# Kernel tuning notes

Measured on AMD Instinct MI355X. Metric: run time of the kernel, lower is better.

## Reference

```python
import jax, jax.numpy as jnp
import numpy as np

B, H, SEQLEN, HEAD_DIM = 1, 16, 4096, 64
SCALE = 1.0 / float(np.sqrt(HEAD_DIM))


def setup_inputs() -> dict:
    key = jax.random.key(0)
    kq, kk, kv = jax.random.split(key, 3)
    q = jax.random.normal(kq, (B, H, SEQLEN, HEAD_DIM), dtype=jnp.float32)
    k = jax.random.normal(kk, (B, H, HEAD_DIM, SEQLEN), dtype=jnp.float32)  # pre-transposed
    v = jax.random.normal(kv, (B, H, SEQLEN, HEAD_DIM), dtype=jnp.float32)
    return {"q": q, "k": k, "v": v}


def reference(q, k, v):
    # causal additive mask: -inf strictly above the diagonal
    mask = jnp.where(
        jnp.triu(jnp.ones((SEQLEN, SEQLEN), dtype=bool), k=1),
        jnp.float32(-jnp.inf), jnp.float32(0.0),
    ).astype(q.dtype)
    scores = jnp.einsum('bhsd,bhdt->bhst', q, k) * SCALE + mask  # [B,H,S,S]
    row_max = jnp.max(scores, axis=-1, keepdims=True)
    p_exp = jnp.exp(scores - row_max)
    denom = jnp.sum(p_exp, axis=-1, keepdims=True)
    p = p_exp / denom                                            # softmax probs
    out = jnp.einsum('bhst,bhtd->bhsd', p, v)                    # [B,H,S,D]
    row_sum = jnp.sum(p, axis=2)                                 # per-key accumulated attention [B,H,S]
    return (out, row_sum)
```

## Files before the change

kernel.cpp:

```cpp
#include <hip/hip_runtime.h>
#include <hip/hip_bf16.h>

#define HEADS 16
#define SEQ   4096
#define DIM   64
#define QT    64
#define KT    64
#define SCALE 0.125f
#define CF    0.18033688011112042f
#define LOG2E 1.4426950408889634f

typedef __bf16 v8bf  __attribute__((ext_vector_type(8)));
typedef __bf16 v4bf  __attribute__((ext_vector_type(4)));
typedef float  f32x4 __attribute__((ext_vector_type(4)));

__device__ __forceinline__ __bf16 to_bf(float f) { return (__bf16)f; }
__device__ __forceinline__ float ex2(float x) { return __builtin_amdgcn_exp2f(x); }
__device__ __forceinline__ float lg2(float x) { return __builtin_amdgcn_logf(x); }

__device__ __forceinline__ void gload16(const __bf16* g, __bf16* l) {
    __builtin_amdgcn_global_load_lds(
        (const __attribute__((address_space(1))) void*)g,
        (__attribute__((address_space(3))) void*)l,
        16, 0, 0);
}

__global__ __launch_bounds__(256) void conv_fused_kernel(
    const float* __restrict__ qg, const float* __restrict__ kg,
    const float* __restrict__ vg, __bf16* __restrict__ Qb,
    __bf16* __restrict__ Kb, __bf16* __restrict__ Vb)
{
    __shared__ __bf16 ldsT[64][65];
    const int h   = blockIdx.y;
    const int t0  = blockIdx.x * 64;
    const int tid = threadIdx.x;
    const int rr  = tid >> 2;
    const int cq  = (tid & 3) * 16;

    if (blockIdx.z == 2) {
        const float* src = qg + ((size_t)h * SEQ + t0 + rr) * DIM + cq;
        __bf16* dst = Qb + ((size_t)h * SEQ + t0 + rr) * DIM + cq;
        v8bf o0, o1;
        #pragma unroll
        for (int j = 0; j < 2; ++j) {
            float4 f0 = *(const float4*)(src + 8 * j);
            float4 f1 = *(const float4*)(src + 8 * j + 4);
            v8bf o;
            o[0] = to_bf(f0.x * CF); o[1] = to_bf(f0.y * CF);
            o[2] = to_bf(f0.z * CF); o[3] = to_bf(f0.w * CF);
            o[4] = to_bf(f1.x * CF); o[5] = to_bf(f1.y * CF);
            o[6] = to_bf(f1.z * CF); o[7] = to_bf(f1.w * CF);
            if (j == 0) o0 = o; else o1 = o;
        }
        *(v8bf*)dst = o0;
        *(v8bf*)(dst + 8) = o1;
        return;
    }

    if (blockIdx.z == 0) {
        const float* src = kg + ((size_t)h * DIM + rr) * SEQ + t0 + cq;
        #pragma unroll
        for (int j = 0; j < 4; ++j) {
            float4 f = *(const float4*)(src + 4 * j);
            ldsT[rr][cq + 4 * j + 0] = to_bf(f.x);
            ldsT[rr][cq + 4 * j + 1] = to_bf(f.y);
            ldsT[rr][cq + 4 * j + 2] = to_bf(f.z);
            ldsT[rr][cq + 4 * j + 3] = to_bf(f.w);
        }
        __syncthreads();
        __bf16* dst = Kb + (size_t)h * SEQ * DIM + (size_t)(t0 + rr) * DIM + cq;
        v8bf o0, o1;
        #pragma unroll
        for (int i = 0; i < 8; ++i) {
            o0[i] = ldsT[cq + i][rr];
            o1[i] = ldsT[cq + 8 + i][rr];
        }
        *(v8bf*)dst = o0;
        *(v8bf*)(dst + 8) = o1;
    } else {
        const float* src = vg + ((size_t)h * SEQ + t0 + rr) * DIM + cq;
        #pragma unroll
        for (int j = 0; j < 4; ++j) {
            float4 f = *(const float4*)(src + 4 * j);
            ldsT[rr][cq + 4 * j + 0] = to_bf(f.x);
            ldsT[rr][cq + 4 * j + 1] = to_bf(f.y);
            ldsT[rr][cq + 4 * j + 2] = to_bf(f.z);
            ldsT[rr][cq + 4 * j + 3] = to_bf(f.w);
        }
        __syncthreads();
        __bf16* dst0 = Vb + ((size_t)h * DIM + rr) * SEQ + t0;
        const int n  = cq >> 4;
        const int c0 = 32 * (n >> 1) + 4 * (n & 1);
        #pragma unroll
        for (int j2 = 0; j2 < 4; ++j2) {
            v4bf ch;
            #pragma unroll
            for (int r = 0; r < 4; ++r)
                ch[r] = ldsT[cq + 4 * j2 + r][rr];
            *(v4bf*)(dst0 + c0 + 8 * j2) = ch;
        }
    }
}

__global__ __launch_bounds__(256, 2) void fa_fwd2_kernel(
    const __bf16* __restrict__ Qb, const __bf16* __restrict__ Kb,
    const __bf16* __restrict__ Vb, float* __restrict__ outg,
    float* __restrict__ lseg)
{
    const int b    = blockIdx.x;
    const int xcd  = b & 7;
    const int j    = b >> 3;
    const int h    = 2 * xcd + (j & 1);
    const int a    = j >> 1;
    const int tid  = threadIdx.x;
    const int wave = tid >> 6;
    const int lane = tid & 63;
    const int g    = lane >> 4;
    const int l16  = lane & 15;
    const int wit  = wave * 16 + l16;

    const int na  = a + 1;
    const int nb  = 64 - a;
    const int nIt = (nb + 1) >> 1;

    __shared__ alignas(16) __bf16 ldsK[2][2][KT * DIM];
    __shared__ alignas(16) __bf16 ldsV[2][2][DIM * KT];

    const int r0 = tid >> 3;
    const int c0 = tid & 7;
    const size_t kOff0 = (size_t)r0 * DIM + (size_t)((c0 ^ (r0 & 7)) << 3);
    const size_t kOff1 = (size_t)(r0 + 32) * DIM + (size_t)((c0 ^ ((r0 + 32) & 7)) << 3);
    const size_t vOff0 = (size_t)r0 * SEQ + (size_t)((c0 ^ (r0 & 7)) << 3);
    const size_t vOff1 = (size_t)(r0 + 32) * SEQ + (size_t)((c0 ^ ((r0 + 32) & 7)) << 3);
    const __bf16* KbH = Kb + (size_t)h * SEQ * DIM;
    const __bf16* VbH = Vb + (size_t)h * DIM * SEQ;
    const int ldsW = wave * 512;

    const int qlo = a * QT + wit;
    const int qhi = (63 - a) * QT + wit;

    const __bf16* qlr = Qb + ((size_t)h * SEQ + qlo) * DIM + g * 8;
    const __bf16* qhr = Qb + ((size_t)h * SEQ + qhi) * DIM + g * 8;
    v8bf aqlo0 = *(const v8bf*)qlr;
    v8bf aqlo1 = *(const v8bf*)(qlr + 32);
    v8bf aqhi0 = *(const v8bf*)qhr;
    v8bf aqhi1 = *(const v8bf*)(qhr + 32);

    f32x4 accl[4], acch[4];
    #pragma unroll
    for (int n = 0; n < 4; ++n) {
        accl[n] = (f32x4){0.f, 0.f, 0.f, 0.f};
        acch[n] = (f32x4){0.f, 0.f, 0.f, 0.f};
    }
    float lpl[4] = {0.f, 0.f, 0.f, 0.f};
    float lph[4] = {0.f, 0.f, 0.f, 0.f};

    int cur = 0;
    #pragma unroll
    for (int u = 0; u < 2; ++u) {
        const __bf16* kb = KbH + (size_t)(64 * u) * DIM;
        const __bf16* vb = VbH + 64 * u;
        gload16(kb + kOff0, &ldsK[0][u][ldsW]);
        gload16(kb + kOff1, &ldsK[0][u][2048 + ldsW]);
        gload16(vb + vOff0, &ldsV[0][u][ldsW]);
        gload16(vb + vOff1, &ldsV[0][u][2048 + ldsW]);
    }
    __syncthreads();

    auto sub_full = [&](int u, int t) {
        f32x4 sl[4], sh[4];
        #pragma unroll
        for (int n = 0; n < 4; ++n) {
            sl[n] = (f32x4){0.f, 0.f, 0.f, 0.f};
            sh[n] = (f32x4){0.f, 0.f, 0.f, 0.f};
        }
        __builtin_amdgcn_s_setprio(1);
        #pragma unroll
        for (int kk = 0; kk < 2; ++kk) {
            #pragma unroll
            for (int n = 0; n < 4; ++n) {
                int row  = 16 * n + l16;
                int byte = row * 128 + kk * 64 + g * 16;
                byte ^= (row & 7) << 4;
                v8bf ak = *(const v8bf*)&ldsK[cur][u][byte >> 1];
                sl[n] = __builtin_amdgcn_mfma_f32_16x16x32_bf16(
                    ak, kk ? aqlo1 : aqlo0, sl[n], 0, 0, 0);
                sh[n] = __builtin_amdgcn_mfma_f32_16x16x32_bf16(
                    ak, kk ? aqhi1 : aqhi0, sh[n], 0, 0, 0);
            }
        }
        __builtin_amdgcn_s_setprio(0);
        if (t >= na - 1) {
            const int lim = (a - t) * 64 + wit;
            #pragma unroll
            for (int n = 0; n < 4; ++n)
                #pragma unroll
                for (int r = 0; r < 4; ++r)
                    if (16 * n + 4 * g + r > lim) sl[n][r] = -3.0e38f;
        }
        v8bf pl0, pl1, ph0, ph1;
        #pragma unroll
        for (int n = 0; n < 4; ++n) {
            #pragma unroll
            for (int r = 0; r < 4; ++r) {
                float p = ex2(sl[n][r]);
                float q = ex2(sh[n][r]);
                lpl[r] += p;
                lph[r] += q;
                if (n < 2) { pl0[(n & 1) * 4 + r] = to_bf(p);
                             ph0[(n & 1) * 4 + r] = to_bf(q); }
                else       { pl1[(n & 1) * 4 + r] = to_bf(p);
                             ph1[(n & 1) * 4 + r] = to_bf(q); }
            }
        }
        __builtin_amdgcn_s_setprio(1);
        #pragma unroll
        for (int kk = 0; kk < 2; ++kk) {
            #pragma unroll
            for (int n = 0; n < 4; ++n) {
                int row  = 16 * n + l16;
                int byte = row * 128 + kk * 64 + g * 16;
                byte ^= (row & 7) << 4;
                v8bf av = *(const v8bf*)&ldsV[cur][u][byte >> 1];
                accl[n] = __builtin_amdgcn_mfma_f32_16x16x32_bf16(
                    av, kk ? pl1 : pl0, accl[n], 0, 0, 0);
                acch[n] = __builtin_amdgcn_mfma_f32_16x16x32_bf16(
                    av, kk ? ph1 : ph0, acch[n], 0, 0, 0);
            }
        }
        __builtin_amdgcn_s_setprio(0);
    };

    auto sub_hi = [&](int u, int t) {
        f32x4 sh[4];
        #pragma unroll
        for (int n = 0; n < 4; ++n) sh[n] = (f32x4){0.f, 0.f, 0.f, 0.f};
        __builtin_amdgcn_s_setprio(1);
        #pragma unroll
        for (int kk = 0; kk < 2; ++kk) {
            #pragma unroll
            for (int n = 0; n < 4; ++n) {
                int row  = 16 * n + l16;
                int byte = row * 128 + kk * 64 + g * 16;
                byte ^= (row & 7) << 4;
                v8bf ak = *(const v8bf*)&ldsK[cur][u][byte >> 1];
                sh[n] = __builtin_amdgcn_mfma_f32_16x16x32_bf16(
                    ak, kk ? aqhi1 : aqhi0, sh[n], 0, 0, 0);
            }
        }
        __builtin_amdgcn_s_setprio(0);
        if (t >= nb - 1) {
            const int lim = (63 - a - t) * 64 + wit;
            #pragma unroll
            for (int n = 0; n < 4; ++n)
                #pragma unroll
                for (int r = 0; r < 4; ++r)
                    if (16 * n + 4 * g + r > lim) sh[n][r] = -3.0e38f;
        }
        v8bf ph0, ph1;
        #pragma unroll
        for (int n = 0; n < 4; ++n) {
            #pragma unroll
            for (int r = 0; r < 4; ++r) {
                float q = ex2(sh[n][r]);
                lph[r] += q;
                if (n < 2) ph0[(n & 1) * 4 + r] = to_bf(q);
                else       ph1[(n & 1) * 4 + r] = to_bf(q);
            }
        }
        __builtin_amdgcn_s_setprio(1);
        #pragma unroll
        for (int kk = 0; kk < 2; ++kk) {
            #pragma unroll
            for (int n = 0; n < 4; ++n) {
                int row  = 16 * n + l16;
                int byte = row * 128 + kk * 64 + g * 16;
                byte ^= (row & 7) << 4;
                v8bf av = *(const v8bf*)&ldsV[cur][u][byte >> 1];
                acch[n] = __builtin_amdgcn_mfma_f32_16x16x32_bf16(
                    av, kk ? ph1 : ph0, acch[n], 0, 0, 0);
            }
        }
        __builtin_amdgcn_s_setprio(0);
    };

    #pragma unroll 1
    for (int it = 0; it < nIt; ++it) {
        if (it + 1 < nIt) {
            #pragma unroll
            for (int u = 0; u < 2; ++u) {
                const __bf16* kb = KbH + (size_t)(128 * (it + 1) + 64 * u) * DIM;
                const __bf16* vb = VbH + 128 * (it + 1) + 64 * u;
                gload16(kb + kOff0, &ldsK[cur ^ 1][u][ldsW]);
                gload16(kb + kOff1, &ldsK[cur ^ 1][u][2048 + ldsW]);
                gload16(vb + vOff0, &ldsV[cur ^ 1][u][ldsW]);
                gload16(vb + vOff1, &ldsV[cur ^ 1][u][2048 + ldsW]);
            }
        }
        const int t0 = 2 * it;
        if (t0 < na) { sub_full(0, t0); sub_full(1, t0 + 1); }
        else         { sub_hi(0, t0);   sub_hi(1, t0 + 1);   }
        __syncthreads();
        cur ^= 1;
    }

    {
        float l = (lpl[0] + lpl[1]) + (lpl[2] + lpl[3]);
        l += __shfl_xor(l, 16);
        l += __shfl_xor(l, 32);
        const float inv = 1.0f / l;
        float* orow = outg + ((size_t)h * SEQ + qlo) * DIM;
        #pragma unroll
        for (int n = 0; n < 4; ++n) {
            f32x4 o = accl[n];
            o[0] *= inv; o[1] *= inv; o[2] *= inv; o[3] *= inv;
            *(f32x4*)(orow + 16 * n + 4 * g) = o;
        }
        if (g == 0) lseg[h * SEQ + qlo] = lg2(l);
    }
    {
        float l = (lph[0] + lph[1]) + (lph[2] + lph[3]);
        l += __shfl_xor(l, 16);
        l += __shfl_xor(l, 32);
        const float inv = 1.0f / l;
        float* orow = outg + ((size_t)h * SEQ + qhi) * DIM;
        #pragma unroll
        for (int n = 0; n < 4; ++n) {
            f32x4 o = acch[n];
            o[0] *= inv; o[1] *= inv; o[2] *= inv; o[3] *= inv;
            *(f32x4*)(orow + 16 * n + 4 * g) = o;
        }
        if (g == 0) lseg[h * SEQ + qhi] = lg2(l);
    }
}

__global__ __launch_bounds__(256, 2) void fa_colsum2_kernel(
    const __bf16* __restrict__ Qb, const __bf16* __restrict__ Kb,
    const float* __restrict__ lseg, float* __restrict__ rsg)
{
    const int b    = blockIdx.x;
    const int xcd  = b & 7;
    const int j    = b >> 3;
    const int h    = 2 * xcd + (j & 1);
    const int ta   = j >> 1;
    const int tb   = 63 - ta;
    const int tid  = threadIdx.x;
    const int wave = tid >> 6;
    const int lane = tid & 63;
    const int g    = lane >> 4;
    const int l16  = lane & 15;

    __shared__ alignas(16) __bf16 ldsK2[2][KT * DIM];
    __shared__ float cs[2][4][KT];

    const int r0 = tid >> 3;
    const int c0 = tid & 7;
    const size_t kOff0 = (size_t)r0 * DIM + (size_t)((c0 ^ (r0 & 7)) << 3);
    const size_t kOff1 = (size_t)(r0 + 32) * DIM + (size_t)((c0 ^ ((r0 + 32) & 7)) << 3);
    const __bf16* KbH = Kb + (size_t)h * SEQ * DIM;
    const int ldsW = wave * 512;

    gload16(KbH + (size_t)ta * KT * DIM + kOff0, &ldsK2[0][ldsW]);
    gload16(KbH + (size_t)ta * KT * DIM + kOff1, &ldsK2[0][2048 + ldsW]);
    gload16(KbH + (size_t)tb * KT * DIM + kOff0, &ldsK2[1][ldsW]);
    gload16(KbH + (size_t)tb * KT * DIM + kOff1, &ldsK2[1][2048 + ldsW]);
    __syncthreads();

    float accA[4] = {0.f, 0.f, 0.f, 0.f};
    float accB[4] = {0.f, 0.f, 0.f, 0.f};

    #pragma unroll 1
    for (int qt = ta; qt < SEQ / QT; ++qt) {
        const int qw = qt * QT + wave * 16;
        const __bf16* qrow = Qb + ((size_t)h * SEQ + qw + l16) * DIM + g * 8;
        v8bf aq0 = *(const v8bf*)qrow;
        v8bf aq1 = *(const v8bf*)(qrow + 32);
        float4 lse4 = *(const float4*)(lseg + (size_t)h * SEQ + qw + 4 * g);

        {
            f32x4 s[4];
            #pragma unroll
            for (int n = 0; n < 4; ++n) s[n] = (f32x4){0.f, 0.f, 0.f, 0.f};
            __builtin_amdgcn_s_setprio(1);
            #pragma unroll
            for (int kk = 0; kk < 2; ++kk)
                #pragma unroll
                for (int n = 0; n < 4; ++n) {
                    int row  = 16 * n + l16;
                    int byte = row * 128 + kk * 64 + g * 16;
                    byte ^= (row & 7) << 4;
                    v8bf bk = *(const v8bf*)&ldsK2[0][byte >> 1];
                    s[n] = __builtin_amdgcn_mfma_f32_16x16x32_bf16(
                        kk ? aq1 : aq0, bk, s[n], 0, 0, 0);
                }
            __builtin_amdgcn_s_setprio(0);
            if (qt == ta) {
                #pragma unroll
                for (int n = 0; n < 4; ++n) {
                    const int key = ta * KT + 16 * n + l16;
                    #pragma unroll
                    for (int r = 0; r < 4; ++r) {
                        float e = ex2(s[n][r] - lse4[r]);
                        accA[n] += (key <= qw + 4 * g + r) ? e : 0.f;
                    }
                }
            } else {
                #pragma unroll
                for (int n = 0; n < 4; ++n)
                    #pragma unroll
                    for (int r = 0; r < 4; ++r)
                        accA[n] += ex2(s[n][r] - lse4[r]);
            }
        }
        if (qt >= tb) {
            f32x4 s[4];
            #pragma unroll
            for (int n = 0; n < 4; ++n) s[n] = (f32x4){0.f, 0.f, 0.f, 0.f};
            __builtin_amdgcn_s_setprio(1);
            #pragma unroll
            for (int kk = 0; kk < 2; ++kk)
                #pragma unroll
                for (int n = 0; n < 4; ++n) {
                    int row  = 16 * n + l16;
                    int byte = row * 128 + kk * 64 + g * 16;
                    byte ^= (row & 7) << 4;
                    v8bf bk = *(const v8bf*)&ldsK2[1][byte >> 1];
                    s[n] = __builtin_amdgcn_mfma_f32_16x16x32_bf16(
                        kk ? aq1 : aq0, bk, s[n], 0, 0, 0);
                }
            __builtin_amdgcn_s_setprio(0);
            if (qt == tb) {
                #pragma unroll
                for (int n = 0; n < 4; ++n) {
                    const int key = tb * KT + 16 * n + l16;
                    #pragma unroll
                    for (int r = 0; r < 4; ++r) {
                        float e = ex2(s[n][r] - lse4[r]);
                        accB[n] += (key <= qw + 4 * g + r) ? e : 0.f;
                    }
                }
            } else {
                #pragma unroll
                for (int n = 0; n < 4; ++n)
                    #pragma unroll
                    for (int r = 0; r < 4; ++r)
                        accB[n] += ex2(s[n][r] - lse4[r]);
            }
        }
    }

    #pragma unroll
    for (int n = 0; n < 4; ++n) {
        accA[n] += __shfl_xor(accA[n], 16);
        accA[n] += __shfl_xor(accA[n], 32);
        accB[n] += __shfl_xor(accB[n], 16);
        accB[n] += __shfl_xor(accB[n], 32);
    }
    if (lane < 16) {
        #pragma unroll
        for (int n = 0; n < 4; ++n) {
            cs[0][wave][16 * n + lane] = accA[n];
            cs[1][wave][16 * n + lane] = accB[n];
        }
    }
    __syncthreads();
    if (tid < KT) {
        rsg[(size_t)h * SEQ + ta * KT + tid] =
            cs[0][0][tid] + cs[0][1][tid] + cs[0][2][tid] + cs[0][3][tid];
    } else if (tid < 2 * KT) {
        const int t = tid - KT;
        rsg[(size_t)h * SEQ + tb * KT + t] =
            cs[1][0][t] + cs[1][1][t] + cs[1][2][t] + cs[1][3][t];
    }
}

__global__ __launch_bounds__(256, 1) void fa_fwd_v1_kernel(
    const float* __restrict__ qg, const float* __restrict__ kg,
    const float* __restrict__ vg, float* __restrict__ outg,
    float* __restrict__ lseg)
{
    const int h    = blockIdx.y;
    const int q0   = blockIdx.x * QT;
    const int tid  = threadIdx.x;
    const int wave = tid >> 6;
    const int lane = tid & 63;
    const int g    = lane >> 4;
    const int l16  = lane & 15;

    __shared__ alignas(16) __bf16 ldsK[KT * DIM];
    __shared__ alignas(16) __bf16 ldsV[DIM * KT];
    __shared__ alignas(16) __bf16 ldsP[4][16 * 72];

    const int qw = q0 + wave * 16;
    v8bf aq[2];
    {
        const float* qrow = qg + ((size_t)h * SEQ + qw + l16) * DIM;
        #pragma unroll
        for (int kk = 0; kk < 2; ++kk) {
            const float* p = qrow + kk * 32 + g * 8;
            float4 f0 = *(const float4*)p;
            float4 f1 = *(const float4*)(p + 4);
            aq[kk][0] = to_bf(f0.x); aq[kk][1] = to_bf(f0.y);
            aq[kk][2] = to_bf(f0.z); aq[kk][3] = to_bf(f0.w);
            aq[kk][4] = to_bf(f1.x); aq[kk][5] = to_bf(f1.y);
            aq[kk][6] = to_bf(f1.z); aq[kk][7] = to_bf(f1.w);
        }
    }
    f32x4 acc[4];
    #pragma unroll
    for (int n = 0; n < 4; ++n) acc[n] = (f32x4){0.f, 0.f, 0.f, 0.f};
    float m_r[4], l_r[4];
    #pragma unroll
    for (int r = 0; r < 4; ++r) { m_r[r] = -__builtin_inff(); l_r[r] = 0.f; }

    const int ntiles = q0 / KT + 1;
    const int kd = tid >> 2;
    const int kc = (tid & 3) * 16;

    for (int t = 0; t < ntiles; ++t) {
        const int t0 = t * KT;
        __syncthreads();
        {
            const float* src = kg + ((size_t)h * DIM + kd) * SEQ + t0 + kc;
            #pragma unroll
            for (int j = 0; j < 4; ++j) {
                float4 f = *(const float4*)(src + 4 * j);
                #pragma unroll
                for (int i = 0; i < 4; ++i) {
                    int row  = kc + 4 * j + i;
                    int byte = row * 128 + kd * 2;
                    byte ^= (row & 7) << 4;
                    ldsK[byte >> 1] = to_bf(((const float*)&f)[i]);
                }
            }
        }
        {
            const float* src = vg + ((size_t)h * SEQ + t0 + kd) * DIM + kc;
            #pragma unroll
            for (int j = 0; j < 4; ++j) {
                float4 f = *(const float4*)(src + 4 * j);
                #pragma unroll
                for (int i = 0; i < 4; ++i) {
                    int row  = kc + 4 * j + i;
                    int byte = row * 128 + kd * 2;
                    byte ^= (row & 7) << 4;
                    ldsV[byte >> 1] = to_bf(((const float*)&f)[i]);
                }
            }
        }
        __syncthreads();

        f32x4 s[4];
        #pragma unroll
        for (int n = 0; n < 4; ++n) s[n] = (f32x4){0.f, 0.f, 0.f, 0.f};
        #pragma unroll
        for (int kk = 0; kk < 2; ++kk)
            #pragma unroll
            for (int n = 0; n < 4; ++n) {
                int row  = 16 * n + l16;
                int byte = row * 128 + kk * 64 + g * 16;
                byte ^= (row & 7) << 4;
                v8bf bk = *(const v8bf*)&ldsK[byte >> 1];
                s[n] = __builtin_amdgcn_mfma_f32_16x16x32_bf16(aq[kk], bk, s[n], 0, 0, 0);
            }
        float pvv[4][4];
        #pragma unroll
        for (int r = 0; r < 4; ++r) {
            const int qq = qw + 4 * g + r;
            float sv[4];
            #pragma unroll
            for (int n = 0; n < 4; ++n) {
                int key = t0 + 16 * n + l16;
                sv[n] = (key <= qq) ? s[n][r] * (SCALE * LOG2E) : -3.0e38f;
            }
            float mx = fmaxf(fmaxf(sv[0], sv[1]), fmaxf(sv[2], sv[3]));
            mx = fmaxf(mx, __shfl_xor(mx, 1));
            mx = fmaxf(mx, __shfl_xor(mx, 2));
            mx = fmaxf(mx, __shfl_xor(mx, 4));
            mx = fmaxf(mx, __shfl_xor(mx, 8));
            float mnew = fmaxf(m_r[r], mx);
            float corr = ex2(m_r[r] - mnew);
            m_r[r] = mnew;
            float rs = 0.f;
            #pragma unroll
            for (int n = 0; n < 4; ++n) {
                float p = (sv[n] > -1.0e38f) ? ex2(sv[n] - mnew) : 0.f;
                pvv[n][r] = p;
                rs += p;
            }
            rs += __shfl_xor(rs, 1);
            rs += __shfl_xor(rs, 2);
            rs += __shfl_xor(rs, 4);
            rs += __shfl_xor(rs, 8);
            l_r[r] = l_r[r] * corr + rs;
            #pragma unroll
            for (int n = 0; n < 4; ++n) acc[n][r] *= corr;
        }
        #pragma unroll
        for (int n = 0; n < 4; ++n)
            #pragma unroll
            for (int r = 0; r < 4; ++r)
                ldsP[wave][(4 * g + r) * 72 + 16 * n + l16] = to_bf(pvv[n][r]);
        asm volatile("s_waitcnt lgkmcnt(0)" ::: "memory");
        __builtin_amdgcn_sched_barrier(0);
        #pragma unroll
        for (int kk = 0; kk < 2; ++kk) {
            v8bf ap = *(const v8bf*)&ldsP[wave][l16 * 72 + 32 * kk + 8 * g];
            #pragma unroll
            for (int n = 0; n < 4; ++n) {
                int row  = 16 * n + l16;
                int byte = row * 128 + kk * 64 + g * 16;
                byte ^= (row & 7) << 4;
                v8bf bv = *(const v8bf*)&ldsV[byte >> 1];
                acc[n] = __builtin_amdgcn_mfma_f32_16x16x32_bf16(ap, bv, acc[n], 0, 0, 0);
            }
        }
    }
    #pragma unroll
    for (int r = 0; r < 4; ++r) {
        const int qq  = qw + 4 * g + r;
        const float inv = 1.0f / l_r[r];
        float* orow = outg + ((size_t)h * SEQ + qq) * DIM;
        #pragma unroll
        for (int n = 0; n < 4; ++n)
            orow[16 * n + l16] = acc[n][r] * inv;
        if (l16 == 0)
            lseg[h * SEQ + qq] = m_r[r] + lg2(l_r[r]);
    }
}

__global__ __launch_bounds__(256, 1) void fa_colsum_v1_kernel(
    const float* __restrict__ qg, const float* __restrict__ kg,
    const float* __restrict__ lseg, float* __restrict__ rsg)
{
    const int h    = blockIdx.y;
    const int t0   = blockIdx.x * KT;
    const int tid  = threadIdx.x;
    const int wave = tid >> 6;
    const int lane = tid & 63;
    const int g    = lane >> 4;
    const int l16  = lane & 15;

    __shared__ alignas(16) __bf16 ldsK[KT * DIM];
    __shared__ float cs[4][KT];
    {
        const int kd = tid >> 2;
        const int kc = (tid & 3) * 16;
        const float* src = kg + ((size_t)h * DIM + kd) * SEQ + t0 + kc;
        #pragma unroll
        for (int j = 0; j < 4; ++j) {
            float4 f = *(const float4*)(src + 4 * j);
            #pragma unroll
            for (int i = 0; i < 4; ++i) {
                int row  = kc + 4 * j + i;
                int byte = row * 128 + kd * 2;
                byte ^= (row & 7) << 4;
                ldsK[byte >> 1] = to_bf(((const float*)&f)[i]);
            }
        }
    }
    __syncthreads();
    float colacc[4] = {0.f, 0.f, 0.f, 0.f};
    for (int qt = t0 / QT; qt < SEQ / QT; ++qt) {
        const int qw = qt * QT + wave * 16;
        const float* qrow = qg + ((size_t)h * SEQ + qw + l16) * DIM;
        v8bf aq[2];
        #pragma unroll
        for (int kk = 0; kk < 2; ++kk) {
            const float* p = qrow + kk * 32 + g * 8;
            float4 f0 = *(const float4*)p;
            float4 f1 = *(const float4*)(p + 4);
            aq[kk][0] = to_bf(f0.x); aq[kk][1] = to_bf(f0.y);
            aq[kk][2] = to_bf(f0.z); aq[kk][3] = to_bf(f0.w);
            aq[kk][4] = to_bf(f1.x); aq[kk][5] = to_bf(f1.y);
            aq[kk][6] = to_bf(f1.z); aq[kk][7] = to_bf(f1.w);
        }
        float lse_r[4];
        #pragma unroll
        for (int r = 0; r < 4; ++r)
            lse_r[r] = lseg[h * SEQ + qw + 4 * g + r];
        f32x4 s[4];
        #pragma unroll
        for (int n = 0; n < 4; ++n) s[n] = (f32x4){0.f, 0.f, 0.f, 0.f};
        #pragma unroll
        for (int kk = 0; kk < 2; ++kk)
            #pragma unroll
            for (int n = 0; n < 4; ++n) {
                int row  = 16 * n + l16;
                int byte = row * 128 + kk * 64 + g * 16;
                byte ^= (row & 7) << 4;
                v8bf bk = *(const v8bf*)&ldsK[byte >> 1];
                s[n] = __builtin_amdgcn_mfma_f32_16x16x32_bf16(aq[kk], bk, s[n], 0, 0, 0);
            }
        #pragma unroll
        for (int n = 0; n < 4; ++n) {
            const int key = t0 + 16 * n + l16;
            #pragma unroll
            for (int r = 0; r < 4; ++r) {
                const int qq = qw + 4 * g + r;
                if (key <= qq)
                    colacc[n] += ex2(s[n][r] * (SCALE * LOG2E) - lse_r[r]);
            }
        }
    }
    #pragma unroll
    for (int n = 0; n < 4; ++n) {
        colacc[n] += __shfl_xor(colacc[n], 16);
        colacc[n] += __shfl_xor(colacc[n], 32);
    }
    if (lane < 16) {
        #pragma unroll
        for (int n = 0; n < 4; ++n)
            cs[wave][16 * n + lane] = colacc[n];
    }
    __syncthreads();
    if (tid < KT) {
        float v = cs[0][tid] + cs[1][tid] + cs[2][tid] + cs[3][tid];
        rsg[h * SEQ + t0 + tid] = v;
    }
}

extern "C" void kernel_launch(void* const* d_in, const int* in_sizes, int n_in,
                              void* d_out, int out_size, void* d_ws, size_t ws_size,
                              hipStream_t stream) {
    (void)in_sizes; (void)n_in; (void)out_size;
    const float* qg = (const float*)d_in[0];
    const float* kg = (const float*)d_in[1];
    const float* vg = (const float*)d_in[2];
    float* outg = (float*)d_out;
    float* rsg  = outg + (size_t)HEADS * SEQ * DIM;

    const size_t nElem   = (size_t)HEADS * SEQ * DIM;
    const size_t lseB    = (size_t)HEADS * SEQ * sizeof(float);
    const size_t needB   = lseB + 3 * nElem * sizeof(__bf16);

    if (ws_size >= needB) {
        float*  lseg = (float*)d_ws;
        __bf16* Qb = (__bf16*)((char*)d_ws + lseB);
        __bf16* Kb = Qb + nElem;
        __bf16* Vb = Kb + nElem;
        conv_fused_kernel<<<dim3(SEQ / 64, HEADS, 3), 256, 0, stream>>>(
            qg, kg, vg, Qb, Kb, Vb);
        fa_fwd2_kernel<<<dim3(512), 256, 0, stream>>>(Qb, Kb, Vb, outg, lseg);
        fa_colsum2_kernel<<<dim3(512), 256, 0, stream>>>(Qb, Kb, lseg, rsg);
    } else {
        float* lseg = (float*)d_ws;
        dim3 grid(SEQ / QT, HEADS);
        fa_fwd_v1_kernel<<<grid, 256, 0, stream>>>(qg, kg, vg, outg, lseg);
        fa_colsum_v1_kernel<<<grid, 256, 0, stream>>>(qg, kg, lseg, rsg);
    }
}
```

Before: 99.99 us.

## Split key tiles across two wave groups in forward kernel with LDS reduction

The forward kernel moves from 4 to 8 waves per block. The two wave groups each process alternate 64-key tiles of the same 128-key chunk instead of one group handling both sequentially. Partial output accumulators and row sums are exchanged through LDS and combined at the end, with each group writing one of the two query tiles. This aims to raise parallelism and occupancy per CU, at the cost of an extra LDS reduction, a barrier, and tighter register limits from the 512-thread launch bound.

```diff
diff --git a/kernel.cpp b/kernel.cpp
--- a/kernel.cpp
+++ b/kernel.cpp
@@ -102,7 +102,7 @@
     }
 }
 
-__global__ __launch_bounds__(256, 2) void fa_fwd2_kernel(
+__global__ __launch_bounds__(512, 4) void fa_fwd8_kernel(
     const __bf16* __restrict__ Qb, const __bf16* __restrict__ Kb,
     const __bf16* __restrict__ Vb, float* __restrict__ outg,
     float* __restrict__ lseg)
@@ -117,30 +117,29 @@
     const int lane = tid & 63;
     const int g    = lane >> 4;
     const int l16  = lane & 15;
-    const int wit  = wave * 16 + l16;
-
-    const int na  = a + 1;
-    const int nb  = 64 - a;
-    const int nIt = (nb + 1) >> 1;
-
-    __shared__ alignas(16) __bf16 ldsK[2][2][KT * DIM];
-    __shared__ alignas(16) __bf16 ldsV[2][2][DIM * KT];
+    const int grp  = wave >> 2;
+    const int w4   = wave & 3;
+    const int wit  = w4 * 16 + l16;
+
+    const int qlo = a;
+    const int qhi = 63 - a;
+    const int NT  = 64 - a;
+    const int nIt = (NT + 1) >> 1;
+
+    __shared__ alignas(16) __bf16 ldsPool[32768];
 
     const int r0 = tid >> 3;
     const int c0 = tid & 7;
-    const size_t kOff0 = (size_t)r0 * DIM + (size_t)((c0 ^ (r0 & 7)) << 3);
-    const size_t kOff1 = (size_t)(r0 + 32) * DIM + (size_t)((c0 ^ ((r0 + 32) & 7)) << 3);
-    const size_t vOff0 = (size_t)r0 * SEQ + (size_t)((c0 ^ (r0 & 7)) << 3);
-    const size_t vOff1 = (size_t)(r0 + 32) * SEQ + (size_t)((c0 ^ ((r0 + 32) & 7)) << 3);
+    const size_t kOff = (size_t)r0 * DIM + (size_t)((c0 ^ (r0 & 7)) << 3);
+    const size_t vOff = (size_t)r0 * SEQ + (size_t)((c0 ^ (r0 & 7)) << 3);
     const __bf16* KbH = Kb + (size_t)h * SEQ * DIM;
     const __bf16* VbH = Vb + (size_t)h * DIM * SEQ;
     const int ldsW = wave * 512;
 
-    const int qlo = a * QT + wit;
-    const int qhi = (63 - a) * QT + wit;
-
-    const __bf16* qlr = Qb + ((size_t)h * SEQ + qlo) * DIM + g * 8;
-    const __bf16* qhr = Qb + ((size_t)h * SEQ + qhi) * DIM + g * 8;
+    const int qLoRow = qlo * QT + wit;
+    const int qHiRow = qhi * QT + wit;
+    const __bf16* qlr = Qb + ((size_t)h * SEQ + qLoRow) * DIM + g * 8;
+    const __bf16* qhr = Qb + ((size_t)h * SEQ + qHiRow) * DIM + g * 8;
     v8bf aqlo0 = *(const v8bf*)qlr;
     v8bf aqlo1 = *(const v8bf*)(qlr + 32);
     v8bf aqhi0 = *(const v8bf*)qhr;
@@ -158,180 +157,207 @@
     int cur = 0;
     #pragma unroll
     for (int u = 0; u < 2; ++u) {
-        const __bf16* kb = KbH + (size_t)(64 * u) * DIM;
-        const __bf16* vb = VbH + 64 * u;
-        gload16(kb + kOff0, &ldsK[0][u][ldsW]);
-        gload16(kb + kOff1, &ldsK[0][u][2048 + ldsW]);
-        gload16(vb + vOff0, &ldsV[0][u][ldsW]);
-        gload16(vb + vOff1, &ldsV[0][u][2048 + ldsW]);
+        gload16(KbH + (size_t)(64 * u) * DIM + kOff,
+                ldsPool + (size_t)u * 4096 + ldsW);
+        gload16(VbH + 64 * u + vOff,
+                ldsPool + 16384 + (size_t)u * 4096 + ldsW);
     }
     __syncthreads();
-
-    auto sub_full = [&](int u, int t) {
-        f32x4 sl[4], sh[4];
-        #pragma unroll
-        for (int n = 0; n < 4; ++n) {
-            sl[n] = (f32x4){0.f, 0.f, 0.f, 0.f};
-            sh[n] = (f32x4){0.f, 0.f, 0.f, 0.f};
-        }
-        __builtin_amdgcn_s_setprio(1);
-        #pragma unroll
-        for (int kk = 0; kk < 2; ++kk) {
-            #pragma unroll
-            for (int n = 0; n < 4; ++n) {
-                int row  = 16 * n + l16;
-                int byte = row * 128 + kk * 64 + g * 16;
-                byte ^= (row & 7) << 4;
-                v8bf ak = *(const v8bf*)&ldsK[cur][u][byte >> 1];
-                sl[n] = __builtin_amdgcn_mfma_f32_16x16x32_bf16(
-                    ak, kk ? aqlo1 : aqlo0, sl[n], 0, 0, 0);
-                sh[n] = __builtin_amdgcn_mfma_f32_16x16x32_bf16(
-                    ak, kk ? aqhi1 : aqhi0, sh[n], 0, 0, 0);
-            }
-        }
-        __builtin_amdgcn_s_setprio(0);
-        if (t >= na - 1) {
-            const int lim = (a - t) * 64 + wit;
-            #pragma unroll
-            for (int n = 0; n < 4; ++n)
-                #pragma unroll
-                for (int r = 0; r < 4; ++r)
-                    if (16 * n + 4 * g + r > lim) sl[n][r] = -3.0e38f;
-        }
-        v8bf pl0, pl1, ph0, ph1;
-        #pragma unroll
-        for (int n = 0; n < 4; ++n) {
-            #pragma unroll
-            for (int r = 0; r < 4; ++r) {
-                float p = ex2(sl[n][r]);
-                float q = ex2(sh[n][r]);
-                lpl[r] += p;
-                lph[r] += q;
-                if (n < 2) { pl0[(n & 1) * 4 + r] = to_bf(p);
-                             ph0[(n & 1) * 4 + r] = to_bf(q); }
-                else       { pl1[(n & 1) * 4 + r] = to_bf(p);
-                             ph1[(n & 1) * 4 + r] = to_bf(q); }
-            }
-        }
-        __builtin_amdgcn_s_setprio(1);
-        #pragma unroll
-        for (int kk = 0; kk < 2; ++kk) {
-            #pragma unroll
-            for (int n = 0; n < 4; ++n) {
-                int row  = 16 * n + l16;
-                int byte = row * 128 + kk * 64 + g * 16;
-                byte ^= (row & 7) << 4;
-                v8bf av = *(const v8bf*)&ldsV[cur][u][byte >> 1];
-                accl[n] = __builtin_amdgcn_mfma_f32_16x16x32_bf16(
-                    av, kk ? pl1 : pl0, accl[n], 0, 0, 0);
-                acch[n] = __builtin_amdgcn_mfma_f32_16x16x32_bf16(
-                    av, kk ? ph1 : ph0, acch[n], 0, 0, 0);
-            }
-        }
-        __builtin_amdgcn_s_setprio(0);
-    };
-
-    auto sub_hi = [&](int u, int t) {
-        f32x4 sh[4];
-        #pragma unroll
-        for (int n = 0; n < 4; ++n) sh[n] = (f32x4){0.f, 0.f, 0.f, 0.f};
-        __builtin_amdgcn_s_setprio(1);
-        #pragma unroll
-        for (int kk = 0; kk < 2; ++kk) {
-            #pragma unroll
-            for (int n = 0; n < 4; ++n) {
-                int row  = 16 * n + l16;
-                int byte = row * 128 + kk * 64 + g * 16;
-                byte ^= (row & 7) << 4;
-                v8bf ak = *(const v8bf*)&ldsK[cur][u][byte >> 1];
-                sh[n] = __builtin_amdgcn_mfma_f32_16x16x32_bf16(
-                    ak, kk ? aqhi1 : aqhi0, sh[n], 0, 0, 0);
-            }
-        }
-        __builtin_amdgcn_s_setprio(0);
-        if (t >= nb - 1) {
-            const int lim = (63 - a - t) * 64 + wit;
-            #pragma unroll
-            for (int n = 0; n < 4; ++n)
-                #pragma unroll
-                for (int r = 0; r < 4; ++r)
-                    if (16 * n + 4 * g + r > lim) sh[n][r] = -3.0e38f;
-        }
-        v8bf ph0, ph1;
-        #pragma unroll
-        for (int n = 0; n < 4; ++n) {
-            #pragma unroll
-            for (int r = 0; r < 4; ++r) {
-                float q = ex2(sh[n][r]);
-                lph[r] += q;
-                if (n < 2) ph0[(n & 1) * 4 + r] = to_bf(q);
-                else       ph1[(n & 1) * 4 + r] = to_bf(q);
-            }
-        }
-        __builtin_amdgcn_s_setprio(1);
-        #pragma unroll
-        for (int kk = 0; kk < 2; ++kk) {
-            #pragma unroll
-            for (int n = 0; n < 4; ++n) {
-                int row  = 16 * n + l16;
-                int byte = row * 128 + kk * 64 + g * 16;
-                byte ^= (row & 7) << 4;
-                v8bf av = *(const v8bf*)&ldsV[cur][u][byte >> 1];
-                acch[n] = __builtin_amdgcn_mfma_f32_16x16x32_bf16(
-                    av, kk ? ph1 : ph0, acch[n], 0, 0, 0);
-            }
-        }
-        __builtin_amdgcn_s_setprio(0);
-    };
 
     #pragma unroll 1
     for (int it = 0; it < nIt; ++it) {
         if (it + 1 < nIt) {
+            const int nbuf = cur ^ 1;
             #pragma unroll
             for (int u = 0; u < 2; ++u) {
-                const __bf16* kb = KbH + (size_t)(128 * (it + 1) + 64 * u) * DIM;
-                const __bf16* vb = VbH + 128 * (it + 1) + 64 * u;
-                gload16(kb + kOff0, &ldsK[cur ^ 1][u][ldsW]);
-                gload16(kb + kOff1, &ldsK[cur ^ 1][u][2048 + ldsW]);
-                gload16(vb + vOff0, &ldsV[cur ^ 1][u][ldsW]);
-                gload16(vb + vOff1, &ldsV[cur ^ 1][u][2048 + ldsW]);
-            }
-        }
-        const int t0 = 2 * it;
-        if (t0 < na) { sub_full(0, t0); sub_full(1, t0 + 1); }
-        else         { sub_hi(0, t0);   sub_hi(1, t0 + 1);   }
+                gload16(KbH + (size_t)(128 * (it + 1) + 64 * u) * DIM + kOff,
+                        ldsPool + (size_t)(nbuf * 2 + u) * 4096 + ldsW);
+                gload16(VbH + (128 * (it + 1) + 64 * u) + vOff,
+                        ldsPool + 16384 + (size_t)(nbuf * 2 + u) * 4096 + ldsW);
+            }
+        }
+        const int t = 2 * it + grp;
+        if (t <= qhi) {
+            const __bf16* Kt = ldsPool + (size_t)(cur * 2 + grp) * 4096;
+            const __bf16* Vt = ldsPool + 16384 + (size_t)(cur * 2 + grp) * 4096;
+            if (t <= qlo) {
+                f32x4 sl[4], sh[4];
+                #pragma unroll
+                for (int n = 0; n < 4; ++n) {
+                    sl[n] = (f32x4){0.f, 0.f, 0.f, 0.f};
+                    sh[n] = (f32x4){0.f, 0.f, 0.f, 0.f};
+                }
+                __builtin_amdgcn_s_setprio(1);
+                #pragma unroll
+                for (int kk = 0; kk < 2; ++kk) {
+                    #pragma unroll
+                    for (int n = 0; n < 4; ++n) {
+                        int row  = 16 * n + l16;
+                        int byte = row * 128 + kk * 64 + g * 16;
+                        byte ^= (row & 7) << 4;
+                        v8bf ak = *(const v8bf*)&Kt[byte >> 1];
+                        sl[n] = __builtin_amdgcn_mfma_f32_16x16x32_bf16(
+                            ak, kk ? aqlo1 : aqlo0, sl[n], 0, 0, 0);
+                        sh[n] = __builtin_amdgcn_mfma_f32_16x16x32_bf16(
+                            ak, kk ? aqhi1 : aqhi0, sh[n], 0, 0, 0);
+                    }
+                }
+                __builtin_amdgcn_s_setprio(0);
+                if (t == qlo) {
+                    #pragma unroll
+                    for (int n = 0; n < 4; ++n)
+                        #pragma unroll
+                        for (int r = 0; r < 4; ++r)
+                            if (16 * n + 4 * g + r > wit) sl[n][r] = -3.0e38f;
+                }
+                v8bf pl0, pl1, ph0, ph1;
+                #pragma unroll
+                for (int n = 0; n < 4; ++n) {
+                    #pragma unroll
+                    for (int r = 0; r < 4; ++r) {
+                        float p = ex2(sl[n][r]);
+                        float q = ex2(sh[n][r]);
+                        lpl[r] += p;
+                        lph[r] += q;
+                        if (n < 2) { pl0[(n & 1) * 4 + r] = to_bf(p);
+                                     ph0[(n & 1) * 4 + r] = to_bf(q); }
+                        else       { pl1[(n & 1) * 4 + r] = to_bf(p);
+                                     ph1[(n & 1) * 4 + r] = to_bf(q); }
+                    }
+                }
+                __builtin_amdgcn_s_setprio(1);
+                #pragma unroll
+                for (int kk = 0; kk < 2; ++kk) {
+                    #pragma unroll
+                    for (int n = 0; n < 4; ++n) {
+                        int row  = 16 * n + l16;
+                        int byte = row * 128 + kk * 64 + g * 16;
+                        byte ^= (row & 7) << 4;
+                        v8bf av = *(const v8bf*)&Vt[byte >> 1];
+                        accl[n] = __builtin_amdgcn_mfma_f32_16x16x32_bf16(
+                            av, kk ? pl1 : pl0, accl[n], 0, 0, 0);
+                        acch[n] = __builtin_amdgcn_mfma_f32_16x16x32_bf16(
+                            av, kk ? ph1 : ph0, acch[n], 0, 0, 0);
+                    }
+                }
+                __builtin_amdgcn_s_setprio(0);
+            } else {
+                f32x4 sh[4];
+                #pragma unroll
+                for (int n = 0; n < 4; ++n) sh[n] = (f32x4){0.f, 0.f, 0.f, 0.f};
+                __builtin_amdgcn_s_setprio(1);
+                #pragma unroll
+                for (int kk = 0; kk < 2; ++kk) {
+                    #pragma unroll
+                    for (int n = 0; n < 4; ++n) {
+                        int row  = 16 * n + l16;
+                        int byte = row * 128 + kk * 64 + g * 16;
+                        byte ^= (row & 7) << 4;
+                        v8bf ak = *(const v8bf*)&Kt[byte >> 1];
+                        sh[n] = __builtin_amdgcn_mfma_f32_16x16x32_bf16(
+                            ak, kk ? aqhi1 : aqhi0, sh[n], 0, 0, 0);
+                    }
+                }
+                __builtin_amdgcn_s_setprio(0);
+                if (t == qhi) {
+                    #pragma unroll
+                    for (int n = 0; n < 4; ++n)
+                        #pragma unroll
+                        for (int r = 0; r < 4; ++r)
+                            if (16 * n + 4 * g + r > wit) sh[n][r] = -3.0e38f;
+                }
+                v8bf ph0, ph1;
+                #pragma unroll
+                for (int n = 0; n < 4; ++n) {
+                    #pragma unroll
+                    for (int r = 0; r < 4; ++r) {
+                        float q = ex2(sh[n][r]);
+                        lph[r] += q;
+                        if (n < 2) ph0[(n & 1) * 4 + r] = to_bf(q);
+                        else       ph1[(n & 1) * 4 + r] = to_bf(q);
+                    }
+                }
+                __builtin_amdgcn_s_setprio(1);
+                #pragma unroll
+                for (int kk = 0; kk < 2; ++kk) {
+                    #pragma unroll
+                    for (int n = 0; n < 4; ++n) {
+                        int row  = 16 * n + l16;
+                        int byte = row * 128 + kk * 64 + g * 16;
+                        byte ^= (row & 7) << 4;
+                        v8bf av = *(const v8bf*)&Vt[byte >> 1];
+                        acch[n] = __builtin_amdgcn_mfma_f32_16x16x32_bf16(
+                            av, kk ? ph1 : ph0, acch[n], 0, 0, 0);
+                    }
+                }
+                __builtin_amdgcn_s_setprio(0);
+            }
+        }
         __syncthreads();
         cur ^= 1;
     }
 
+    float* scratch = (float*)ldsPool;
     {
-        float l = (lpl[0] + lpl[1]) + (lpl[2] + lpl[3]);
-        l += __shfl_xor(l, 16);
-        l += __shfl_xor(l, 32);
-        const float inv = 1.0f / l;
-        float* orow = outg + ((size_t)h * SEQ + qlo) * DIM;
-        #pragma unroll
-        for (int n = 0; n < 4; ++n) {
-            f32x4 o = accl[n];
-            o[0] *= inv; o[1] *= inv; o[2] *= inv; o[3] *= inv;
-            *(f32x4*)(orow + 16 * n + 4 * g) = o;
-        }
-        if (g == 0) lseg[h * SEQ + qlo] = lg2(l);
-    }
+        float* sp = scratch + (size_t)(grp ? (4 + w4) : w4) * 1280;
+        if (grp == 0) {
+            #pragma unroll
+            for (int n = 0; n < 4; ++n)
+                #pragma unroll
+                for (int r = 0; r < 4; ++r)
+                    sp[(n * 4 + r) * 64 + lane] = acch[n][r];
+            #pragma unroll
+            for (int r = 0; r < 4; ++r) sp[(16 + r) * 64 + lane] = lph[r];
+        } else {
+            #pragma unroll
+            for (int n = 0; n < 4; ++n)
+                #pragma unroll
+                for (int r = 0; r < 4; ++r)
+                    sp[(n * 4 + r) * 64 + lane] = accl[n][r];
+            #pragma unroll
+            for (int r = 0; r < 4; ++r) sp[(16 + r) * 64 + lane] = lpl[r];
+        }
+    }
+    __syncthreads();
+    f32x4 accO[4];
+    float lpO[4];
     {
-        float l = (lph[0] + lph[1]) + (lph[2] + lph[3]);
-        l += __shfl_xor(l, 16);
-        l += __shfl_xor(l, 32);
-        const float inv = 1.0f / l;
-        float* orow = outg + ((size_t)h * SEQ + qhi) * DIM;
-        #pragma unroll
-        for (int n = 0; n < 4; ++n) {
-            f32x4 o = acch[n];
-            o[0] *= inv; o[1] *= inv; o[2] *= inv; o[3] *= inv;
-            *(f32x4*)(orow + 16 * n + 4 * g) = o;
-        }
-        if (g == 0) lseg[h * SEQ + qhi] = lg2(l);
-    }
+        const float* op = scratch + (size_t)(grp ? w4 : (4 + w4)) * 1280;
+        if (grp == 0) {
+            #pragma unroll
+            for (int n = 0; n < 4; ++n)
+                #pragma unroll
+                for (int r = 0; r < 4; ++r)
+                    accO[n][r] = accl[n][r] + op[(n * 4 + r) * 64 + lane];
+            #pragma unroll
+            for (int r = 0; r < 4; ++r)
+                lpO[r] = lpl[r] + op[(16 + r) * 64 + lane];
+        } else {
+            #pragma unroll
+            for (int n = 0; n < 4; ++n)
+                #pragma unroll
+                for (int r = 0; r < 4; ++r)
+                    accO[n][r] = acch[n][r] + op[(n * 4 + r) * 64 + lane];
+            #pragma unroll
+            for (int r = 0; r < 4; ++r)
+                lpO[r] = lph[r] + op[(16 + r) * 64 + lane];
+        }
+    }
+
+    const int q = (grp ? qhi : qlo) * QT + wit;
+    float l = (lpO[0] + lpO[1]) + (lpO[2] + lpO[3]);
+    l += __shfl_xor(l, 16);
+    l += __shfl_xor(l, 32);
+    const float inv = 1.0f / l;
+    float* orow = outg + ((size_t)h * SEQ + q) * DIM;
+    #pragma unroll
+    for (int n = 0; n < 4; ++n) {
+        f32x4 o = accO[n];
+        o[0] *= inv; o[1] *= inv; o[2] *= inv; o[3] *= inv;
+        *(f32x4*)(orow + 16 * n + 4 * g) = o;
+    }
+    if (g == 0)
+        lseg[h * SEQ + q] = lg2(l);
 }
 
 __global__ __launch_bounds__(256, 2) void fa_colsum2_kernel(
@@ -741,7 +767,7 @@
         __bf16* Vb = Kb + nElem;
         conv_fused_kernel<<<dim3(SEQ / 64, HEADS, 3), 256, 0, stream>>>(
             qg, kg, vg, Qb, Kb, Vb);
-        fa_fwd2_kernel<<<dim3(512), 256, 0, stream>>>(Qb, Kb, Vb, outg, lseg);
+        fa_fwd8_kernel<<<dim3(512), 512, 0, stream>>>(Qb, Kb, Vb, outg, lseg);
         fa_colsum2_kernel<<<dim3(512), 256, 0, stream>>>(Qb, Kb, lseg, rsg);
     } else {
         float* lseg = (float*)d_ws;
```

New measurement: 95.89 us. 1.04x faster.
